# Kernel optimization log

Hardware: AMD Instinct MI355X
Metric: run time of the kernel (lower is better)

The kernel has to match this reference:

```python
import jax, jax.numpy as jnp
import numpy as np

EPS = 1e-5
SLOPE = 0.01  # nn.LeakyReLU default


def _subm_conv(feats, W, nbr):
    # feats: [N_in, Cin]; W: [K, Cin, Cout]; nbr: [K, N_out] with sentinel N_in -> zero
    padded = jnp.concatenate([feats, jnp.zeros((1, feats.shape[1]), feats.dtype)], axis=0)
    g = padded[nbr]  # [K, N_out, Cin] gather (rulebook gather stage)
    return jnp.einsum('knc,kcd->nd', g, W)  # GEMM + scatter-accumulate over offsets


def _lrelu(x):
    return jnp.where(x >= 0, x, SLOPE * x)


def _bn(x, gamma, beta):
    # BatchNorm1d in training mode: batch stats over point dim, biased variance
    m = jnp.mean(x, axis=0)
    v = jnp.mean(jnp.square(x - m), axis=0)
    return (x - m) * jax.lax.rsqrt(v + EPS) * gamma + beta


def setup_inputs() -> dict:
    key = jax.random.key(0)
    ks = jax.random.split(key, 12)
    N_in, N_out, Cin, Cout = 80000, 200000, 128, 64
    inp = {
        'x_feats': jax.random.normal(ks[0], (N_in, Cin), jnp.float32),
        'skip_feats': jax.random.normal(ks[1], (N_out, Cout), jnp.float32),
        'nbr_trans': jax.random.randint(ks[2], (27, N_in), 0, N_in + 1, jnp.int32),
        'nbr_up': jax.random.randint(ks[3], (27, N_out), 0, N_in + 1, jnp.int32),
        'nbr1': jax.random.randint(ks[4], (9, N_out), 0, N_out + 1, jnp.int32),
        'nbr2': jax.random.randint(ks[5], (9, N_out), 0, N_out + 1, jnp.int32),
        'nbr3': jax.random.randint(ks[6], (27, N_out), 0, N_out + 1, jnp.int32),
        'W_trans': jax.random.normal(ks[7], (27, Cin, Cout), jnp.float32) * 0.05,
        'W_up': jax.random.normal(ks[8], (27, Cout, Cout), jnp.float32) * 0.05,
        'W1': jax.random.normal(ks[9], (9, Cout, Cout), jnp.float32) * 0.05,
        'W2': jax.random.normal(ks[10], (9, Cout, Cout), jnp.float32) * 0.05,
        'W3': jax.random.normal(ks[11], (27, Cout, Cout), jnp.float32) * 0.05,
        'gamma_t': jnp.ones((Cout,), jnp.float32), 'beta_t': jnp.zeros((Cout,), jnp.float32),
        'gamma1': jnp.ones((Cout,), jnp.float32), 'beta1': jnp.zeros((Cout,), jnp.float32),
        'gamma2': jnp.ones((Cout,), jnp.float32), 'beta2': jnp.zeros((Cout,), jnp.float32),
        'gamma3': jnp.ones((Cout,), jnp.float32), 'beta3': jnp.zeros((Cout,), jnp.float32),
    }
    return inp


def reference(x_feats, skip_feats, nbr_trans, nbr_up, nbr1, nbr2, nbr3,
              W_trans, W_up, W1, W2, W3,
              gamma_t, beta_t, gamma1, beta1, gamma2, beta2, gamma3, beta3):
    # trans_dilao (SubMConv3d 3x3x3) + LeakyReLU + BN
    h = _subm_conv(x_feats, W_trans, nbr_trans)          # [N_in, Cout]
    h = _bn(_lrelu(h), gamma_t, beta_t)
    # SparseInverseConv3d: gather from coarse points into dense output set
    u = _subm_conv(h, W_up, nbr_up)                      # [N_out, Cout]
    u = u + skip_feats                                   # residual skip add
    # conv1 (1x3x3) + act + bn
    e = _bn(_lrelu(_subm_conv(u, W1, nbr1)), gamma1, beta1)
    # conv2 (3x1x3) + act + bn
    e = _bn(_lrelu(_subm_conv(e, W2, nbr2)), gamma2, beta2)
    # conv3 (3x3x3) + act + bn
    e = _bn(_lrelu(_subm_conv(e, W3, nbr3)), gamma3, beta3)
    return e
```

## Files before the change

kernel.cpp:

```cpp
#include <hip/hip_runtime.h>

#define EPS 1e-5f
#define SLOPE 0.01f

typedef __attribute__((ext_vector_type(8))) short bf16x8;
typedef __attribute__((ext_vector_type(4))) float f32x4;

static __device__ __forceinline__ unsigned short f2bf(float f) {
    unsigned u = __float_as_uint(f);
    u += 0x7fff + ((u >> 16) & 1);
    return (unsigned short)(u >> 16);
}
static __device__ __forceinline__ float bf2f(unsigned short h) {
    return __uint_as_float(((unsigned)h) << 16);
}

static __device__ __forceinline__ void gload16(const unsigned short* g, void* l) {
    __builtin_amdgcn_global_load_lds(
        (const __attribute__((address_space(1))) unsigned int*)g,
        (__attribute__((address_space(3))) unsigned int*)l,
        16, 0, 0);
}

template<int K, int NCH>
__global__ __launch_bounds__(256, 3)
void conv_mfma(const unsigned short* __restrict__ in, int tableN,
               const int* __restrict__ nbr, int Nout,
               const unsigned short* __restrict__ Wt2,
               const float* __restrict__ skip,
               unsigned short* __restrict__ out_bf,
               float* __restrict__ out_f32,
               float* __restrict__ stats, int do_lrelu)
{
    constexpr int Cin = NCH * 64;
    constexpr int KT  = K * NCH;

    __shared__ unsigned short Abuf[2][128 * 64];
    __shared__ int   sIdx[K * 128];
    __shared__ float red[2][64][4];

    const int t    = threadIdx.x;
    const int lane = t & 63;
    const int w    = t >> 6;
    const int q    = lane >> 4;
    const int m    = lane & 15;
    const int row0 = blockIdx.x * 128;
    const int wrow = w * 32;

    const int glr = lane >> 3;
    const int gls = lane & 7;

    for (int e = t; e < K * 128; e += 256) {
        int k = e >> 7, r = e & 127;
        int gr = row0 + r;
        sIdx[e] = (gr < Nout) ? nbr[(size_t)k * Nout + gr] : tableN;
    }
    __syncthreads();

    f32x4 acc[2][4];
#pragma unroll
    for (int rt = 0; rt < 2; ++rt)
#pragma unroll
        for (int ct = 0; ct < 4; ++ct) acc[rt][ct] = (f32x4){0.f, 0.f, 0.f, 0.f};

    auto gather = [&](int kk, int p) {
        const int k  = kk / NCH;
        const int cc = kk % NCH;
        const int* sI = &sIdx[k * 128 + wrow];
#pragma unroll
        for (int j = 0; j < 4; ++j) {
            int src = sI[j * 8 + glr];
            const unsigned short* g =
                in + (size_t)src * Cin + cc * 64 + (gls ^ glr) * 8;
            gload16(g, (void*)&Abuf[p][(wrow + j * 8) * 64]);
        }
    };
    auto loadB = [&](int kk, bf16x8 (&bb)[2][4]) {
#pragma unroll
        for (int kc = 0; kc < 2; ++kc)
#pragma unroll
            for (int ct = 0; ct < 4; ++ct)
                bb[kc][ct] = *(const bf16x8*)(
                    Wt2 + (((size_t)(kk * 2 + kc) * 4 + ct) * 64 + lane) * 8);
    };

    bf16x8 bR[2][2][4];
    gather(0, 0);
    loadB(0, bR[0]);
    asm volatile("" ::: "memory");

#pragma unroll
    for (int kk = 0; kk < KT; ++kk) {
        const int p = kk & 1;
        if (kk + 1 < KT) {
            gather(kk + 1, p ^ 1);
            loadB(kk + 1, bR[p ^ 1]);
            asm volatile("s_waitcnt vmcnt(12)" ::: "memory");
        } else {
            asm volatile("s_waitcnt vmcnt(0)" ::: "memory");
        }
        bf16x8 a[2][2];
#pragma unroll
        for (int kc = 0; kc < 2; ++kc)
#pragma unroll
            for (int rt = 0; rt < 2; ++rt)
                a[kc][rt] = *(const bf16x8*)
                    &Abuf[p][(wrow + rt * 16 + m) * 64 +
                             (((kc * 4 + q) ^ (m & 7)) * 8)];
#pragma unroll
        for (int kc = 0; kc < 2; ++kc)
#pragma unroll
            for (int rt = 0; rt < 2; ++rt)
#pragma unroll
                for (int ct = 0; ct < 4; ++ct)
                    acc[rt][ct] = __builtin_amdgcn_mfma_f32_16x16x32_bf16(
                        a[kc][rt], bR[p][kc][ct], acc[rt][ct], 0, 0, 0);
        asm volatile("" ::: "memory");
    }

    float psum[4] = {0.f, 0.f, 0.f, 0.f}, psq[4] = {0.f, 0.f, 0.f, 0.f};
#pragma unroll
    for (int rt = 0; rt < 2; ++rt) {
#pragma unroll
        for (int ct = 0; ct < 4; ++ct) {
            int col = ct * 16 + m;
#pragma unroll
            for (int reg = 0; reg < 4; ++reg) {
                int r = row0 + wrow + rt * 16 + q * 4 + reg;
                if (r < Nout) {
                    float v = acc[rt][ct][reg];
                    if (skip) v += skip[(size_t)r * 64 + col];
                    if (do_lrelu) v = (v >= 0.f) ? v : SLOPE * v;
                    if (out_bf) out_bf[(size_t)r * 64 + col] = f2bf(v);
                    else        out_f32[(size_t)r * 64 + col] = v;
                    psum[ct] += v;
                    psq[ct]  += v * v;
                }
            }
        }
    }

    if (stats) {
#pragma unroll
        for (int ct = 0; ct < 4; ++ct) {
            psum[ct] += __shfl_down(psum[ct], 32);
            psum[ct] += __shfl_down(psum[ct], 16);
            psq[ct]  += __shfl_down(psq[ct], 32);
            psq[ct]  += __shfl_down(psq[ct], 16);
        }
        if (q == 0) {
#pragma unroll
            for (int ct = 0; ct < 4; ++ct) {
                red[0][ct * 16 + m][w] = psum[ct];
                red[1][ct * 16 + m][w] = psq[ct];
            }
        }
        __syncthreads();
        if (t < 64) {
            float s  = red[0][t][0] + red[0][t][1] + red[0][t][2] + red[0][t][3];
            float qq = red[1][t][0] + red[1][t][1] + red[1][t][2] + red[1][t][3];
            atomicAdd(&stats[t], s);
            atomicAdd(&stats[64 + t], qq);
        }
    }
}

__global__ __launch_bounds__(256)
void bn_apply_bf16(unsigned short* __restrict__ buf, size_t total8,
                   const float* __restrict__ stats,
                   const float* __restrict__ gamma,
                   const float* __restrict__ beta, float invN)
{
    __shared__ float sc[64], sh[64];
    int t = threadIdx.x;
    if (t < 64) {
        float mean = stats[t] * invN;
        float var  = stats[64 + t] * invN - mean * mean;
        float s    = gamma[t] * rsqrtf(var + EPS);
        sc[t] = s;
        sh[t] = beta[t] - mean * s;
    }
    __syncthreads();
    for (size_t i = (size_t)blockIdx.x * blockDim.x + t; i < total8;
         i += (size_t)gridDim.x * blockDim.x) {
        int4 v = ((const int4*)buf)[i];
        unsigned short* e = (unsigned short*)&v;
        int c0 = ((int)(i & 7)) << 3;
#pragma unroll
        for (int j = 0; j < 8; ++j)
            e[j] = f2bf(bf2f(e[j]) * sc[c0 + j] + sh[c0 + j]);
        ((int4*)buf)[i] = v;
    }
}

__global__ __launch_bounds__(256)
void bn_apply_f32(float* __restrict__ buf, int N,
                  const float* __restrict__ stats,
                  const float* __restrict__ gamma,
                  const float* __restrict__ beta, float invN)
{
    __shared__ float sc[64], sh[64];
    int t = threadIdx.x;
    if (t < 64) {
        float mean = stats[t] * invN;
        float var  = stats[64 + t] * invN - mean * mean;
        float s    = gamma[t] * rsqrtf(var + EPS);
        sc[t] = s;
        sh[t] = beta[t] - mean * s;
    }
    __syncthreads();
    size_t total4 = (size_t)N * 16;
    for (size_t i = (size_t)blockIdx.x * blockDim.x + t; i < total4;
         i += (size_t)gridDim.x * blockDim.x) {
        float4 v = ((const float4*)buf)[i];
        int c0 = ((int)(i & 15)) << 2;
        v.x = v.x * sc[c0]     + sh[c0];
        v.y = v.y * sc[c0 + 1] + sh[c0 + 1];
        v.z = v.z * sc[c0 + 2] + sh[c0 + 2];
        v.w = v.w * sc[c0 + 3] + sh[c0 + 3];
        ((float4*)buf)[i] = v;
    }
}

__global__ __launch_bounds__(256)
void cvt_bf16(const float* __restrict__ in, unsigned short* __restrict__ out,
              size_t n4)
{
    for (size_t i = (size_t)blockIdx.x * blockDim.x + threadIdx.x; i < n4;
         i += (size_t)gridDim.x * blockDim.x) {
        float4 v = ((const float4*)in)[i];
        ushort4 o;
        o.x = f2bf(v.x); o.y = f2bf(v.y); o.z = f2bf(v.z); o.w = f2bf(v.w);
        ((ushort4*)out)[i] = o;
    }
}

__global__ __launch_bounds__(256)
void zero_sentinels(unsigned short* xb, int Nin128,
                    unsigned short* tb, int Nin64,
                    unsigned short* ub, unsigned short* ab, unsigned short* vb,
                    int Nout64)
{
    int t = threadIdx.x;
    if (t < 128) xb[(size_t)Nin128 + t] = 0;
    if (t < 64) {
        tb[(size_t)Nin64 + t] = 0;
        ub[(size_t)Nout64 + t] = 0;
        ab[(size_t)Nout64 + t] = 0;
        vb[(size_t)Nout64 + t] = 0;
    }
}

static __device__ __forceinline__ void wt2_one(int e, const float* __restrict__ W,
                                               unsigned short* __restrict__ Wt2,
                                               int NCH)
{
    int j  = e & 7;
    int l  = (e >> 3) & 63;
    int ct = (e >> 9) & 3;
    int kc = (e >> 11) & 1;
    int kk = e >> 12;
    int qq = l >> 4, mm = l & 15;
    int k  = kk / NCH, cc = kk % NCH;
    int Cin = NCH * 64;
    int c  = cc * 64 + kc * 32 + qq * 8 + j;
    int d  = ct * 16 + mm;
    Wt2[e] = f2bf(W[((size_t)k * Cin + c) * 64 + d]);
}

__global__ __launch_bounds__(256)
void wt_cvt_all(const float* __restrict__ W_trans, const float* __restrict__ W_up,
                const float* __restrict__ W1, const float* __restrict__ W2,
                const float* __restrict__ W3,
                unsigned short* __restrict__ wt_t, unsigned short* __restrict__ wt_u,
                unsigned short* __restrict__ wt1, unsigned short* __restrict__ wt2,
                unsigned short* __restrict__ wt3)
{
    const int S0 = 27 * 128 * 64;
    const int S1 = 27 * 64 * 64;
    const int S2 = 9 * 64 * 64;
    const int S3 = 9 * 64 * 64;
    const int S4 = 27 * 64 * 64;
    int e = blockIdx.x * blockDim.x + threadIdx.x;
    if (e < S0) { wt2_one(e, W_trans, wt_t, 2); return; }
    e -= S0;
    if (e < S1) { wt2_one(e, W_up, wt_u, 1); return; }
    e -= S1;
    if (e < S2) { wt2_one(e, W1, wt1, 1); return; }
    e -= S2;
    if (e < S3) { wt2_one(e, W2, wt2, 1); return; }
    e -= S3;
    if (e < S4) { wt2_one(e, W3, wt3, 1); }
}

extern "C" void kernel_launch(void* const* d_in, const int* in_sizes, int n_in,
                              void* d_out, int out_size, void* d_ws, size_t ws_size,
                              hipStream_t stream) {
    const float* x_feats   = (const float*)d_in[0];
    const float* skip      = (const float*)d_in[1];
    const int*   nbr_trans = (const int*)d_in[2];
    const int*   nbr_up    = (const int*)d_in[3];
    const int*   nbr1      = (const int*)d_in[4];
    const int*   nbr2      = (const int*)d_in[5];
    const int*   nbr3      = (const int*)d_in[6];
    const float* W_trans   = (const float*)d_in[7];
    const float* W_up      = (const float*)d_in[8];
    const float* W1        = (const float*)d_in[9];
    const float* W2        = (const float*)d_in[10];
    const float* W3        = (const float*)d_in[11];
    const float* gamma_t   = (const float*)d_in[12];
    const float* beta_t    = (const float*)d_in[13];
    const float* gamma1    = (const float*)d_in[14];
    const float* beta1     = (const float*)d_in[15];
    const float* gamma2    = (const float*)d_in[16];
    const float* beta2     = (const float*)d_in[17];
    const float* gamma3    = (const float*)d_in[18];
    const float* beta3     = (const float*)d_in[19];

    const int Nin  = in_sizes[0] / 128;
    const int Nout = in_sizes[1] / 64;

    size_t off = 0;
    auto alloc = [&](size_t bytes) {
        void* p = (char*)d_ws + off;
        off = (off + bytes + 255) & ~(size_t)255;
        return p;
    };
    unsigned short* xb   = (unsigned short*)alloc(((size_t)Nin + 1) * 128 * 2);
    unsigned short* tb   = (unsigned short*)alloc(((size_t)Nin + 1) * 64 * 2);
    unsigned short* ub   = (unsigned short*)alloc(((size_t)Nout + 1) * 64 * 2);
    unsigned short* ab   = (unsigned short*)alloc(((size_t)Nout + 1) * 64 * 2);
    unsigned short* vb   = (unsigned short*)alloc(((size_t)Nout + 1) * 64 * 2);
    unsigned short* wt_t = (unsigned short*)alloc((size_t)27 * 128 * 64 * 2);
    unsigned short* wt_u = (unsigned short*)alloc((size_t)27 * 64 * 64 * 2);
    unsigned short* wt1  = (unsigned short*)alloc((size_t)9 * 64 * 64 * 2);
    unsigned short* wt2  = (unsigned short*)alloc((size_t)9 * 64 * 64 * 2);
    unsigned short* wt3  = (unsigned short*)alloc((size_t)27 * 64 * 64 * 2);
    float* stats = (float*)alloc(512 * sizeof(float));
    float* out   = (float*)d_out;

    hipMemsetAsync(stats, 0, 512 * sizeof(float), stream);

    dim3 blk(256);
    const float invNin  = 1.f / (float)Nin;
    const float invNout = 1.f / (float)Nout;

    wt_cvt_all<<<2016, blk, 0, stream>>>(W_trans, W_up, W1, W2, W3,
                                         wt_t, wt_u, wt1, wt2, wt3);
    cvt_bf16<<<2048, blk, 0, stream>>>(x_feats, xb, (size_t)Nin * 32);
    zero_sentinels<<<1, blk, 0, stream>>>(xb, Nin * 128, tb, Nin * 64,
                                          ub, ab, vb, Nout * 64);

    const int gIn  = (Nin  + 127) / 128;
    const int gOut = (Nout + 127) / 128;

    conv_mfma<27, 2><<<gIn, blk, 0, stream>>>(xb, Nin, nbr_trans, Nin,
                                              wt_t, nullptr, tb, nullptr, stats + 0, 1);
    bn_apply_bf16<<<1024, blk, 0, stream>>>(tb, (size_t)Nin * 8, stats + 0,
                                            gamma_t, beta_t, invNin);
    conv_mfma<27, 1><<<gOut, blk, 0, stream>>>(tb, Nin, nbr_up, Nout,
                                               wt_u, skip, ub, nullptr, nullptr, 0);
    conv_mfma<9, 1><<<gOut, blk, 0, stream>>>(ub, Nout, nbr1, Nout,
                                              wt1, nullptr, ab, nullptr, stats + 128, 1);
    bn_apply_bf16<<<2048, blk, 0, stream>>>(ab, (size_t)Nout * 8, stats + 128,
                                            gamma1, beta1, invNout);
    conv_mfma<9, 1><<<gOut, blk, 0, stream>>>(ab, Nout, nbr2, Nout,
                                              wt2, nullptr, vb, nullptr, stats + 256, 1);
    bn_apply_bf16<<<2048, blk, 0, stream>>>(vb, (size_t)Nout * 8, stats + 256,
                                            gamma2, beta2, invNout);
    conv_mfma<27, 1><<<gOut, blk, 0, stream>>>(vb, Nout, nbr3, Nout,
                                               wt3, nullptr, nullptr, out, stats + 384, 1);
    bn_apply_f32<<<2048, blk, 0, stream>>>(out, Nout, stats + 384,
                                           gamma3, beta3, invNout);
}
```

Measured before the change: 721.3 us.

## Halve conv tile to 64 rows and drop B double-buffering for occupancy

Shrinks each conv block from 128 to 64 output rows, so each wave handles one 16-row MFMA tile instead of two. The weight registers are no longer double-buffered: B fragments are loaded each iteration just before the next gather. The waitcnt drops accordingly and launch bounds rise to 5 blocks per SM. The aim is more resident waves to hide the latency of the random gathers, at the cost of B weights being reloaded with less reuse per block and less prefetch slack for them.

Measured after the change: 843.9 us. 17.0% more time.

```diff
diff --git a/kernel.cpp b/kernel.cpp
--- a/kernel.cpp
+++ b/kernel.cpp
@@ -23,7 +23,7 @@
 }
 
 template<int K, int NCH>
-__global__ __launch_bounds__(256, 3)
+__global__ __launch_bounds__(256, 5)
 void conv_mfma(const unsigned short* __restrict__ in, int tableN,
                const int* __restrict__ nbr, int Nout,
                const unsigned short* __restrict__ Wt2,
@@ -35,8 +35,8 @@
     constexpr int Cin = NCH * 64;
     constexpr int KT  = K * NCH;
 
-    __shared__ unsigned short Abuf[2][128 * 64];
-    __shared__ int   sIdx[K * 128];
+    __shared__ unsigned short Abuf[2][64 * 64];
+    __shared__ int   sIdx[K * 64];
     __shared__ float red[2][64][4];
 
     const int t    = threadIdx.x;
@@ -44,98 +44,84 @@
     const int w    = t >> 6;
     const int q    = lane >> 4;
     const int m    = lane & 15;
-    const int row0 = blockIdx.x * 128;
-    const int wrow = w * 32;
+    const int row0 = blockIdx.x * 64;
+    const int wrow = w * 16;
 
     const int glr = lane >> 3;
     const int gls = lane & 7;
 
-    for (int e = t; e < K * 128; e += 256) {
-        int k = e >> 7, r = e & 127;
+    for (int e = t; e < K * 64; e += 256) {
+        int k = e >> 6, r = e & 63;
         int gr = row0 + r;
         sIdx[e] = (gr < Nout) ? nbr[(size_t)k * Nout + gr] : tableN;
     }
     __syncthreads();
 
-    f32x4 acc[2][4];
-#pragma unroll
-    for (int rt = 0; rt < 2; ++rt)
-#pragma unroll
-        for (int ct = 0; ct < 4; ++ct) acc[rt][ct] = (f32x4){0.f, 0.f, 0.f, 0.f};
+    f32x4 acc[4];
+#pragma unroll
+    for (int ct = 0; ct < 4; ++ct) acc[ct] = (f32x4){0.f, 0.f, 0.f, 0.f};
 
     auto gather = [&](int kk, int p) {
         const int k  = kk / NCH;
         const int cc = kk % NCH;
-        const int* sI = &sIdx[k * 128 + wrow];
-#pragma unroll
-        for (int j = 0; j < 4; ++j) {
+        const int* sI = &sIdx[k * 64 + wrow];
+#pragma unroll
+        for (int j = 0; j < 2; ++j) {
             int src = sI[j * 8 + glr];
             const unsigned short* g =
                 in + (size_t)src * Cin + cc * 64 + (gls ^ glr) * 8;
             gload16(g, (void*)&Abuf[p][(wrow + j * 8) * 64]);
         }
     };
-    auto loadB = [&](int kk, bf16x8 (&bb)[2][4]) {
-#pragma unroll
-        for (int kc = 0; kc < 2; ++kc)
-#pragma unroll
-            for (int ct = 0; ct < 4; ++ct)
-                bb[kc][ct] = *(const bf16x8*)(
-                    Wt2 + (((size_t)(kk * 2 + kc) * 4 + ct) * 64 + lane) * 8);
-    };
-
-    bf16x8 bR[2][2][4];
+
+    bf16x8 bR[2][4];
     gather(0, 0);
-    loadB(0, bR[0]);
     asm volatile("" ::: "memory");
 
 #pragma unroll
     for (int kk = 0; kk < KT; ++kk) {
         const int p = kk & 1;
+#pragma unroll
+        for (int kc = 0; kc < 2; ++kc)
+#pragma unroll
+            for (int ct = 0; ct < 4; ++ct)
+                bR[kc][ct] = *(const bf16x8*)(
+                    Wt2 + (((size_t)(kk * 2 + kc) * 4 + ct) * 64 + lane) * 8);
         if (kk + 1 < KT) {
             gather(kk + 1, p ^ 1);
-            loadB(kk + 1, bR[p ^ 1]);
-            asm volatile("s_waitcnt vmcnt(12)" ::: "memory");
+            asm volatile("s_waitcnt vmcnt(2)" ::: "memory");
         } else {
             asm volatile("s_waitcnt vmcnt(0)" ::: "memory");
         }
-        bf16x8 a[2][2];
+        bf16x8 a[2];
 #pragma unroll
         for (int kc = 0; kc < 2; ++kc)
-#pragma unroll
-            for (int rt = 0; rt < 2; ++rt)
-                a[kc][rt] = *(const bf16x8*)
-                    &Abuf[p][(wrow + rt * 16 + m) * 64 +
-                             (((kc * 4 + q) ^ (m & 7)) * 8)];
+            a[kc] = *(const bf16x8*)
+                &Abuf[p][(wrow + m) * 64 + (((kc * 4 + q) ^ (m & 7)) * 8)];
 #pragma unroll
         for (int kc = 0; kc < 2; ++kc)
 #pragma unroll
-            for (int rt = 0; rt < 2; ++rt)
-#pragma unroll
-                for (int ct = 0; ct < 4; ++ct)
-                    acc[rt][ct] = __builtin_amdgcn_mfma_f32_16x16x32_bf16(
-                        a[kc][rt], bR[p][kc][ct], acc[rt][ct], 0, 0, 0);
+            for (int ct = 0; ct < 4; ++ct)
+                acc[ct] = __builtin_amdgcn_mfma_f32_16x16x32_bf16(
+                    a[kc], bR[kc][ct], acc[ct], 0, 0, 0);
         asm volatile("" ::: "memory");
     }
 
     float psum[4] = {0.f, 0.f, 0.f, 0.f}, psq[4] = {0.f, 0.f, 0.f, 0.f};
 #pragma unroll
-    for (int rt = 0; rt < 2; ++rt) {
-#pragma unroll
-        for (int ct = 0; ct < 4; ++ct) {
-            int col = ct * 16 + m;
-#pragma unroll
-            for (int reg = 0; reg < 4; ++reg) {
-                int r = row0 + wrow + rt * 16 + q * 4 + reg;
-                if (r < Nout) {
-                    float v = acc[rt][ct][reg];
-                    if (skip) v += skip[(size_t)r * 64 + col];
-                    if (do_lrelu) v = (v >= 0.f) ? v : SLOPE * v;
-                    if (out_bf) out_bf[(size_t)r * 64 + col] = f2bf(v);
-                    else        out_f32[(size_t)r * 64 + col] = v;
-                    psum[ct] += v;
-                    psq[ct]  += v * v;
-                }
+    for (int ct = 0; ct < 4; ++ct) {
+        int col = ct * 16 + m;
+#pragma unroll
+        for (int reg = 0; reg < 4; ++reg) {
+            int r = row0 + wrow + q * 4 + reg;
+            if (r < Nout) {
+                float v = acc[ct][reg];
+                if (skip) v += skip[(size_t)r * 64 + col];
+                if (do_lrelu) v = (v >= 0.f) ? v : SLOPE * v;
+                if (out_bf) out_bf[(size_t)r * 64 + col] = f2bf(v);
+                else        out_f32[(size_t)r * 64 + col] = v;
+                psum[ct] += v;
+                psq[ct]  += v * v;
             }
         }
     }
@@ -351,8 +337,8 @@
     zero_sentinels<<<1, blk, 0, stream>>>(xb, Nin * 128, tb, Nin * 64,
                                           ub, ab, vb, Nout * 64);
 
-    const int gIn  = (Nin  + 127) / 128;
-    const int gOut = (Nout + 127) / 128;
+    const int gIn  = (Nin  + 63) / 64;
+    const int gOut = (Nout + 63) / 64;
 
     conv_mfma<27, 2><<<gIn, blk, 0, stream>>>(xb, Nin, nbr_trans, Nin,
                                               wt_t, nullptr, tb, nullptr, stats + 0, 1);
```

## Fuse BatchNorm apply into next conv's gathered-operand load

Applied to the files above, without the earlier changes.

Removes the three standalone bf16 BN-apply passes. Each following conv now applies the per-channel scale and shift to the gathered A fragments in registers before the MFMA. The sentinel row is set to the value that BN maps to zero, -shift/scale, so padded neighbors still contribute nothing. This saves a full read-modify-write pass per BN layer, but adds per-element convert and FMA work inside the MFMA loop, raises register pressure, and double-rounds the sentinel through bf16.

Result: slower. 742.8 us (+3.0%).

```diff
diff --git a/kernel.cpp b/kernel.cpp
--- a/kernel.cpp
+++ b/kernel.cpp
@@ -22,7 +22,7 @@
         16, 0, 0);
 }
 
-template<int K, int NCH>
+template<int K, int NCH, int FUSE>
 __global__ __launch_bounds__(256, 3)
 void conv_mfma(const unsigned short* __restrict__ in, int tableN,
                const int* __restrict__ nbr, int Nout,
@@ -30,7 +30,10 @@
                const float* __restrict__ skip,
                unsigned short* __restrict__ out_bf,
                float* __restrict__ out_f32,
-               float* __restrict__ stats, int do_lrelu)
+               float* __restrict__ stats, int do_lrelu,
+               const float* __restrict__ bn_stats,
+               const float* __restrict__ bn_gamma,
+               const float* __restrict__ bn_beta, float bn_invN)
 {
     constexpr int Cin = NCH * 64;
     constexpr int KT  = K * NCH;
@@ -38,6 +41,7 @@
     __shared__ unsigned short Abuf[2][128 * 64];
     __shared__ int   sIdx[K * 128];
     __shared__ float red[2][64][4];
+    __shared__ float scL[64], shL[64];
 
     const int t    = threadIdx.x;
     const int lane = t & 63;
@@ -55,7 +59,26 @@
         int gr = row0 + r;
         sIdx[e] = (gr < Nout) ? nbr[(size_t)k * Nout + gr] : tableN;
     }
+    if (FUSE && t < 64) {
+        float mean = bn_stats[t] * bn_invN;
+        float var  = bn_stats[64 + t] * bn_invN - mean * mean;
+        float s    = bn_gamma[t] * rsqrtf(var + EPS);
+        scL[t] = s;
+        shL[t] = bn_beta[t] - mean * s;
+    }
     __syncthreads();
+
+    float scR[2][8], shR[2][8];
+    if (FUSE) {
+#pragma unroll
+        for (int kc = 0; kc < 2; ++kc)
+#pragma unroll
+            for (int j = 0; j < 8; ++j) {
+                int c = kc * 32 + q * 8 + j;
+                scR[kc][j] = scL[c];
+                shR[kc][j] = shL[c];
+            }
+    }
 
     f32x4 acc[2][4];
 #pragma unroll
@@ -107,6 +130,18 @@
                 a[kc][rt] = *(const bf16x8*)
                     &Abuf[p][(wrow + rt * 16 + m) * 64 +
                              (((kc * 4 + q) ^ (m & 7)) * 8)];
+        if (FUSE) {
+#pragma unroll
+            for (int kc = 0; kc < 2; ++kc)
+#pragma unroll
+                for (int rt = 0; rt < 2; ++rt)
+#pragma unroll
+                    for (int j = 0; j < 8; ++j) {
+                        float x = bf2f((unsigned short)a[kc][rt][j]);
+                        a[kc][rt][j] =
+                            (short)f2bf(x * scR[kc][j] + shR[kc][j]);
+                    }
+        }
 #pragma unroll
         for (int kc = 0; kc < 2; ++kc)
 #pragma unroll
@@ -165,31 +200,19 @@
     }
 }
 
-__global__ __launch_bounds__(256)
-void bn_apply_bf16(unsigned short* __restrict__ buf, size_t total8,
-                   const float* __restrict__ stats,
-                   const float* __restrict__ gamma,
-                   const float* __restrict__ beta, float invN)
-{
-    __shared__ float sc[64], sh[64];
-    int t = threadIdx.x;
-    if (t < 64) {
-        float mean = stats[t] * invN;
-        float var  = stats[64 + t] * invN - mean * mean;
-        float s    = gamma[t] * rsqrtf(var + EPS);
-        sc[t] = s;
-        sh[t] = beta[t] - mean * s;
-    }
-    __syncthreads();
-    for (size_t i = (size_t)blockIdx.x * blockDim.x + t; i < total8;
-         i += (size_t)gridDim.x * blockDim.x) {
-        int4 v = ((const int4*)buf)[i];
-        unsigned short* e = (unsigned short*)&v;
-        int c0 = ((int)(i & 7)) << 3;
-#pragma unroll
-        for (int j = 0; j < 8; ++j)
-            e[j] = f2bf(bf2f(e[j]) * sc[c0 + j] + sh[c0 + j]);
-        ((int4*)buf)[i] = v;
+__global__ __launch_bounds__(64)
+void set_sentinel_bn(unsigned short* __restrict__ tab, int tableN,
+                     const float* __restrict__ stats,
+                     const float* __restrict__ gamma,
+                     const float* __restrict__ beta, float invN)
+{
+    int c = threadIdx.x;
+    if (c < 64) {
+        float mean = stats[c] * invN;
+        float var  = stats[64 + c] * invN - mean * mean;
+        float s    = gamma[c] * rsqrtf(var + EPS);
+        float sh   = beta[c] - mean * s;
+        tab[(size_t)tableN * 64 + c] = f2bf(-sh / s);
     }
 }
 
@@ -354,22 +377,27 @@
     const int gIn  = (Nin  + 127) / 128;
     const int gOut = (Nout + 127) / 128;
 
-    conv_mfma<27, 2><<<gIn, blk, 0, stream>>>(xb, Nin, nbr_trans, Nin,
-                                              wt_t, nullptr, tb, nullptr, stats + 0, 1);
-    bn_apply_bf16<<<1024, blk, 0, stream>>>(tb, (size_t)Nin * 8, stats + 0,
-                                            gamma_t, beta_t, invNin);
-    conv_mfma<27, 1><<<gOut, blk, 0, stream>>>(tb, Nin, nbr_up, Nout,
-                                               wt_u, skip, ub, nullptr, nullptr, 0);
-    conv_mfma<9, 1><<<gOut, blk, 0, stream>>>(ub, Nout, nbr1, Nout,
-                                              wt1, nullptr, ab, nullptr, stats + 128, 1);
-    bn_apply_bf16<<<2048, blk, 0, stream>>>(ab, (size_t)Nout * 8, stats + 128,
-                                            gamma1, beta1, invNout);
-    conv_mfma<9, 1><<<gOut, blk, 0, stream>>>(ab, Nout, nbr2, Nout,
-                                              wt2, nullptr, vb, nullptr, stats + 256, 1);
-    bn_apply_bf16<<<2048, blk, 0, stream>>>(vb, (size_t)Nout * 8, stats + 256,
-                                            gamma2, beta2, invNout);
-    conv_mfma<27, 1><<<gOut, blk, 0, stream>>>(vb, Nout, nbr3, Nout,
-                                               wt3, nullptr, nullptr, out, stats + 384, 1);
+    conv_mfma<27, 2, 0><<<gIn, blk, 0, stream>>>(
+        xb, Nin, nbr_trans, Nin, wt_t, nullptr, tb, nullptr, stats + 0, 1,
+        nullptr, nullptr, nullptr, 0.f);
+    set_sentinel_bn<<<1, 64, 0, stream>>>(tb, Nin, stats + 0,
+                                          gamma_t, beta_t, invNin);
+    conv_mfma<27, 1, 1><<<gOut, blk, 0, stream>>>(
+        tb, Nin, nbr_up, Nout, wt_u, skip, ub, nullptr, nullptr, 0,
+        stats + 0, gamma_t, beta_t, invNin);
+    conv_mfma<9, 1, 0><<<gOut, blk, 0, stream>>>(
+        ub, Nout, nbr1, Nout, wt1, nullptr, ab, nullptr, stats + 128, 1,
+        nullptr, nullptr, nullptr, 0.f);
+    set_sentinel_bn<<<1, 64, 0, stream>>>(ab, Nout, stats + 128,
+                                          gamma1, beta1, invNout);
+    conv_mfma<9, 1, 1><<<gOut, blk, 0, stream>>>(
+        ab, Nout, nbr2, Nout, wt2, nullptr, vb, nullptr, stats + 256, 1,
+        stats + 128, gamma1, beta1, invNout);
+    set_sentinel_bn<<<1, 64, 0, stream>>>(vb, Nout, stats + 256,
+                                          gamma2, beta2, invNout);
+    conv_mfma<27, 1, 1><<<gOut, blk, 0, stream>>>(
+        vb, Nout, nbr3, Nout, wt3, nullptr, nullptr, out, stats + 384, 1,
+        stats + 256, gamma2, beta2, invNout);
     bn_apply_f32<<<2048, blk, 0, stream>>>(out, Nout, stats + 384,
                                            gamma3, beta3, invNout);
 }
```

## Fold intermediate BatchNorm into next conv weights and bias via sentinel trick

Applied to the files above, without the earlier changes.

Removes the three in-place bf16 BatchNorm apply passes by scaling the next conv's weights by the per-channel BN scale and adding a per-output bias. The BN shift is folded in by writing the sentinel row as -shift/scale, so gathered missing neighbours still contribute zero after the affine fold. A small single-block kernel computes the compensating bias from the scaled weights. Weight conversion now happens after each BN's statistics are ready, which adds small serialized launches and rounding differences from bf16 scaled weights and the bf16 sentinel value.

Result: slower. 788.4 us (+9.3%).

```diff
diff --git a/kernel.cpp b/kernel.cpp
--- a/kernel.cpp
+++ b/kernel.cpp
@@ -30,7 +30,8 @@
                const float* __restrict__ skip,
                unsigned short* __restrict__ out_bf,
                float* __restrict__ out_f32,
-               float* __restrict__ stats, int do_lrelu)
+               float* __restrict__ stats, int do_lrelu,
+               const float* __restrict__ bias)
 {
     constexpr int Cin = NCH * 64;
     constexpr int KT  = K * NCH;
@@ -56,6 +57,12 @@
         sIdx[e] = (gr < Nout) ? nbr[(size_t)k * Nout + gr] : tableN;
     }
     __syncthreads();
+
+    float bsv[4] = {0.f, 0.f, 0.f, 0.f};
+    if (bias) {
+#pragma unroll
+        for (int ct = 0; ct < 4; ++ct) bsv[ct] = bias[ct * 16 + m];
+    }
 
     f32x4 acc[2][4];
 #pragma unroll
@@ -128,7 +135,7 @@
             for (int reg = 0; reg < 4; ++reg) {
                 int r = row0 + wrow + rt * 16 + q * 4 + reg;
                 if (r < Nout) {
-                    float v = acc[rt][ct][reg];
+                    float v = acc[rt][ct][reg] + bsv[ct];
                     if (skip) v += skip[(size_t)r * 64 + col];
                     if (do_lrelu) v = (v >= 0.f) ? v : SLOPE * v;
                     if (out_bf) out_bf[(size_t)r * 64 + col] = f2bf(v);
@@ -166,31 +173,69 @@
 }
 
 __global__ __launch_bounds__(256)
-void bn_apply_bf16(unsigned short* __restrict__ buf, size_t total8,
-                   const float* __restrict__ stats,
-                   const float* __restrict__ gamma,
-                   const float* __restrict__ beta, float invN)
-{
-    __shared__ float sc[64], sh[64];
+void wt_scale(const float* __restrict__ W, unsigned short* __restrict__ Wt2,
+              int total, const float* __restrict__ stats,
+              const float* __restrict__ gamma, float invN)
+{
+    __shared__ float scL[64];
+    int t = threadIdx.x;
+    if (t < 64) {
+        float mean = stats[t] * invN;
+        float var  = stats[64 + t] * invN - mean * mean;
+        scL[t] = gamma[t] * rsqrtf(var + EPS);
+    }
+    __syncthreads();
+    int e = blockIdx.x * blockDim.x + t;
+    if (e >= total) return;
+    int j  = e & 7;
+    int l  = (e >> 3) & 63;
+    int ct = (e >> 9) & 3;
+    int kc = (e >> 11) & 1;
+    int k  = e >> 12;
+    int qq = l >> 4, mm = l & 15;
+    int c  = kc * 32 + qq * 8 + j;
+    int d  = ct * 16 + mm;
+    Wt2[e] = f2bf(W[((size_t)k * 64 + c) * 64 + d] * scL[c]);
+}
+
+template<int K>
+__global__ __launch_bounds__(256)
+void sent_bias(unsigned short* __restrict__ tab, int tableN,
+               const unsigned short* __restrict__ Wt2,
+               float* __restrict__ B,
+               const float* __restrict__ stats,
+               const float* __restrict__ gamma,
+               const float* __restrict__ beta, float invN)
+{
+    __shared__ float sentF[64];
+    __shared__ float redB[4][64];
     int t = threadIdx.x;
     if (t < 64) {
         float mean = stats[t] * invN;
         float var  = stats[64 + t] * invN - mean * mean;
         float s    = gamma[t] * rsqrtf(var + EPS);
-        sc[t] = s;
-        sh[t] = beta[t] - mean * s;
+        float sh   = beta[t] - mean * s;
+        unsigned short sv = f2bf(-sh / s);
+        tab[(size_t)tableN * 64 + t] = sv;
+        sentF[t] = bf2f(sv);
     }
     __syncthreads();
-    for (size_t i = (size_t)blockIdx.x * blockDim.x + t; i < total8;
-         i += (size_t)gridDim.x * blockDim.x) {
-        int4 v = ((const int4*)buf)[i];
-        unsigned short* e = (unsigned short*)&v;
-        int c0 = ((int)(i & 7)) << 3;
-#pragma unroll
-        for (int j = 0; j < 8; ++j)
-            e[j] = f2bf(bf2f(e[j]) * sc[c0 + j] + sh[c0 + j]);
-        ((int4*)buf)[i] = v;
-    }
+    int d    = t & 63;
+    int part = t >> 6;
+    int ct = d >> 4, mm = d & 15;
+    float s = 0.f;
+    for (int k = part; k < K; k += 4) {
+#pragma unroll
+        for (int c = 0; c < 64; ++c) {
+            int kc = c >> 5, qq = (c & 31) >> 3, j = c & 7;
+            int e = ((((k * 2 + kc) * 4 + ct) * 64) + qq * 16 + mm) * 8 + j;
+            s += bf2f(Wt2[e]) * sentF[c];
+        }
+    }
+    redB[part][d] = s;
+    __syncthreads();
+    if (part == 0)
+        B[d] = -(redB[0][d] + redB[1][d] + redB[2][d] + redB[3][d]);
 }
 
 __global__ __launch_bounds__(256)
@@ -269,28 +314,17 @@
 }
 
 __global__ __launch_bounds__(256)
-void wt_cvt_all(const float* __restrict__ W_trans, const float* __restrict__ W_up,
-                const float* __restrict__ W1, const float* __restrict__ W2,
-                const float* __restrict__ W3,
-                unsigned short* __restrict__ wt_t, unsigned short* __restrict__ wt_u,
-                unsigned short* __restrict__ wt1, unsigned short* __restrict__ wt2,
-                unsigned short* __restrict__ wt3)
+void wt_cvt_unscaled(const float* __restrict__ W_trans,
+                     const float* __restrict__ W1,
+                     unsigned short* __restrict__ wt_t,
+                     unsigned short* __restrict__ wt1)
 {
     const int S0 = 27 * 128 * 64;
-    const int S1 = 27 * 64 * 64;
     const int S2 = 9 * 64 * 64;
-    const int S3 = 9 * 64 * 64;
-    const int S4 = 27 * 64 * 64;
     int e = blockIdx.x * blockDim.x + threadIdx.x;
     if (e < S0) { wt2_one(e, W_trans, wt_t, 2); return; }
     e -= S0;
-    if (e < S1) { wt2_one(e, W_up, wt_u, 1); return; }
-    e -= S1;
-    if (e < S2) { wt2_one(e, W1, wt1, 1); return; }
-    e -= S2;
-    if (e < S3) { wt2_one(e, W2, wt2, 1); return; }
-    e -= S3;
-    if (e < S4) { wt2_one(e, W3, wt3, 1); }
+    if (e < S2) { wt2_one(e, W1, wt1, 1); }
 }
 
 extern "C" void kernel_launch(void* const* d_in, const int* in_sizes, int n_in,
@@ -337,6 +371,7 @@
     unsigned short* wt2  = (unsigned short*)alloc((size_t)9 * 64 * 64 * 2);
     unsigned short* wt3  = (unsigned short*)alloc((size_t)27 * 64 * 64 * 2);
     float* stats = (float*)alloc(512 * sizeof(float));
+    float* biasB = (float*)alloc(192 * sizeof(float));
     float* out   = (float*)d_out;
 
     hipMemsetAsync(stats, 0, 512 * sizeof(float), stream);
@@ -345,31 +380,43 @@
     const float invNin  = 1.f / (float)Nin;
     const float invNout = 1.f / (float)Nout;
 
-    wt_cvt_all<<<2016, blk, 0, stream>>>(W_trans, W_up, W1, W2, W3,
-                                         wt_t, wt_u, wt1, wt2, wt3);
+    wt_cvt_unscaled<<<1008, blk, 0, stream>>>(W_trans, W1, wt_t, wt1);
     cvt_bf16<<<2048, blk, 0, stream>>>(x_feats, xb, (size_t)Nin * 32);
     zero_sentinels<<<1, blk, 0, stream>>>(xb, Nin * 128, tb, Nin * 64,
                                           ub, ab, vb, Nout * 64);
 
     const int gIn  = (Nin  + 127) / 128;
     const int gOut = (Nout + 127) / 128;
-
-    conv_mfma<27, 2><<<gIn, blk, 0, stream>>>(xb, Nin, nbr_trans, Nin,
-                                              wt_t, nullptr, tb, nullptr, stats + 0, 1);
-    bn_apply_bf16<<<1024, blk, 0, stream>>>(tb, (size_t)Nin * 8, stats + 0,
-                                            gamma_t, beta_t, invNin);
-    conv_mfma<27, 1><<<gOut, blk, 0, stream>>>(tb, Nin, nbr_up, Nout,
-                                               wt_u, skip, ub, nullptr, nullptr, 0);
-    conv_mfma<9, 1><<<gOut, blk, 0, stream>>>(ub, Nout, nbr1, Nout,
-                                              wt1, nullptr, ab, nullptr, stats + 128, 1);
-    bn_apply_bf16<<<2048, blk, 0, stream>>>(ab, (size_t)Nout * 8, stats + 128,
-                                            gamma1, beta1, invNout);
-    conv_mfma<9, 1><<<gOut, blk, 0, stream>>>(ab, Nout, nbr2, Nout,
-                                              wt2, nullptr, vb, nullptr, stats + 256, 1);
-    bn_apply_bf16<<<2048, blk, 0, stream>>>(vb, (size_t)Nout * 8, stats + 256,
-                                            gamma2, beta2, invNout);
-    conv_mfma<27, 1><<<gOut, blk, 0, stream>>>(vb, Nout, nbr3, Nout,
-                                               wt3, nullptr, nullptr, out, stats + 384, 1);
+    const int W27  = 27 * 64 * 64;
+    const int W9   = 9 * 64 * 64;
+
+    conv_mfma<27, 2><<<gIn, blk, 0, stream>>>(
+        xb, Nin, nbr_trans, Nin, wt_t, nullptr, tb, nullptr, stats + 0, 1,
+        nullptr);
+    wt_scale<<<(W27 + 255) / 256, blk, 0, stream>>>(
+        W_up, wt_u, W27, stats + 0, gamma_t, invNin);
+    sent_bias<27><<<1, blk, 0, stream>>>(tb, Nin, wt_u, biasB + 0,
+                                         stats + 0, gamma_t, beta_t, invNin);
+    conv_mfma<27, 1><<<gOut, blk, 0, stream>>>(
+        tb, Nin, nbr_up, Nout, wt_u, skip, ub, nullptr, nullptr, 0,
+        biasB + 0);
+    conv_mfma<9, 1><<<gOut, blk, 0, stream>>>(
+        ub, Nout, nbr1, Nout, wt1, nullptr, ab, nullptr, stats + 128, 1,
+        nullptr);
+    wt_scale<<<(W9 + 255) / 256, blk, 0, stream>>>(
+        W2, wt2, W9, stats + 128, gamma1, invNout);
+    sent_bias<9><<<1, blk, 0, stream>>>(ab, Nout, wt2, biasB + 64,
+                                        stats + 128, gamma1, beta1, invNout);
+    conv_mfma<9, 1><<<gOut, blk, 0, stream>>>(
+        ab, Nout, nbr2, Nout, wt2, nullptr, vb, nullptr, stats + 256, 1,
+        biasB + 64);
+    wt_scale<<<(W27 + 255) / 256, blk, 0, stream>>>(
+        W3, wt3, W27, stats + 256, gamma2, invNout);
+    sent_bias<27><<<1, blk, 0, stream>>>(vb, Nout, wt3, biasB + 128,
+                                         stats + 256, gamma2, beta2, invNout);
+    conv_mfma<27, 1><<<gOut, blk, 0, stream>>>(
+        vb, Nout, nbr3, Nout, wt3, nullptr, nullptr, out, stats + 384, 1,
+        biasB + 128);
     bn_apply_f32<<<2048, blk, 0, stream>>>(out, Nout, stats + 384,
                                            gamma3, beta3, invNout);
 }
```
